# Kernel tuning notes

Hardware: AMD Instinct MI355X
Metric: run time of the kernel (lower is better)

## Reference

```python
import jax, jax.numpy as jnp
import numpy as np

NUM_HEADS = 8
EMBED_DIM = 128
HEAD_DIM = EMBED_DIM // NUM_HEADS  # 16
NB_FEATURES = EMBED_DIM            # 128
EPS = 1e-4


def _make_projection(nb_rows, nb_cols, rng):
    # gaussian_orthogonal_random_matrix with scaling=0
    blocks = []
    for _ in range(nb_rows // nb_cols):
        q, _ = np.linalg.qr(rng.standard_normal((nb_cols, nb_cols)))
        blocks.append(q.T)
    rem = nb_rows - (nb_rows // nb_cols) * nb_cols
    if rem > 0:
        q, _ = np.linalg.qr(rng.standard_normal((nb_cols, nb_cols)))
        blocks.append(q.T[:rem])
    final = np.concatenate(blocks, axis=0)
    mult = np.linalg.norm(rng.standard_normal((nb_rows, nb_cols)), axis=1)
    return (mult[:, None] * final).astype(np.float32)


def setup_inputs() -> dict:
    key = jax.random.key(0)
    ks = jax.random.split(key, 7)
    R, C, E = 8, 2048, EMBED_DIM
    s = 1.0 / np.sqrt(E)
    x = jax.random.normal(ks[0], (R, C, E), dtype=jnp.float32)
    Wq = jax.random.uniform(ks[1], (E, E), jnp.float32, -s, s)
    bq = jax.random.uniform(ks[2], (E,), jnp.float32, -s, s)
    Wk = jax.random.uniform(ks[3], (E, E), jnp.float32, -s, s)
    bk = jax.random.uniform(ks[4], (E,), jnp.float32, -s, s)
    Wv = jax.random.uniform(ks[5], (E, E), jnp.float32, -s, s)
    bv = jax.random.uniform(ks[6], (E,), jnp.float32, -s, s)
    proj = jnp.asarray(_make_projection(NB_FEATURES, HEAD_DIM, np.random.default_rng(0)))
    return {"x": x, "Wq": Wq, "bq": bq, "Wk": Wk, "bk": bk, "Wv": Wv, "bv": bv, "proj": proj}


def _softmax_kernel(data, proj, is_query):
    # data: (R, h, n, d); proj: (F, d)
    d = data.shape[-1]
    normalizer = d ** (-0.25)
    ratio = proj.shape[0] ** (-0.5)
    data_dash = jnp.einsum('rhnd,jd->rhnj', normalizer * data, proj)  # (R,h,n,F)
    diag = jnp.sum(data * data, axis=-1, keepdims=True) * 0.5 * normalizer ** 2
    if is_query:
        m = jnp.max(data_dash, axis=-1, keepdims=True)
    else:
        m = jnp.max(data_dash, axis=(-1, -2), keepdims=True)
    return ratio * (jnp.exp(data_dash - diag - m) + EPS)


def reference(x, Wq, bq, Wk, bk, Wv, bv, proj):
    R, C, E = x.shape
    h, hd = NUM_HEADS, HEAD_DIM

    def proj_heads(W, b):
        y = jnp.einsum('rce,fe->rcf', x, W) + b
        return y.reshape(R, C, h, hd).transpose(0, 2, 1, 3)  # (R,h,C,hd)

    q = _softmax_kernel(proj_heads(Wq, bq), proj, is_query=True)   # (R,h,C,F)
    k = _softmax_kernel(proj_heads(Wk, bk), proj, is_query=False)  # (R,h,C,F)
    v = proj_heads(Wv, bv)                                          # (R,h,C,hd)

    # fold batch (R) into the feature dim: (h, C, R*F) / (h, C, R*hd)
    qf = q.transpose(1, 2, 0, 3).reshape(h, C, R * NB_FEATURES)
    kf = k.transpose(1, 2, 0, 3).reshape(h, C, R * NB_FEATURES)
    vf = v.transpose(1, 2, 0, 3).reshape(h, C, R * hd)

    k_sum = kf.sum(axis=-2)                                   # (h, D)
    D_inv = 1.0 / jnp.einsum('hnd,hd->hn', qf, k_sum)         # (h, C)
    context = jnp.einsum('hnd,hne->hde', kf, vf)              # (h, D, Ev)
    out = jnp.einsum('hde,hnd,hn->hne', context, qf, D_inv)   # (h, C, R*hd)

    out = out.reshape(h, C, R, hd).transpose(2, 1, 0, 3).reshape(R, C, E)
    attn = jnp.einsum('hqf,hkf->hqk', qf, kf)                 # (h, C, C)
    return out, attn
```

## Files before the change

kernel.cpp:

```cpp
#include <hip/hip_runtime.h>
#include <hip/hip_bf16.h>
#include <stdint.h>

typedef __bf16 bf16x8 __attribute__((ext_vector_type(8)));
typedef float  f32x4  __attribute__((ext_vector_type(4)));

#define RATIO 0.08838834764831845f
#define EPSV  1e-4f

#define GLOBAL_AS __attribute__((address_space(1)))
#define LDS_AS    __attribute__((address_space(3)))

static __device__ __forceinline__ void gload16(const void* g, void* l) {
  __builtin_amdgcn_global_load_lds((GLOBAL_AS const void*)g, (LDS_AS void*)l, 16, 0, 0);
}

static constexpr size_t OFF_XB    = 0;
static constexpr size_t OFF_WCAT  = OFF_XB    + 4194304;
static constexpr size_t OFF_MQ    = OFF_WCAT  + 98304;
static constexpr size_t OFF_MK    = OFF_MQ    + 262144;
static constexpr size_t OFF_BCAT  = OFF_MK    + 262144;
static constexpr size_t OFF_BQF   = OFF_BCAT  + 2048;
static constexpr size_t OFF_BKF   = OFF_BQF   + 4096;
static constexpr size_t OFF_Y     = OFF_BKF   + 4096;
static constexpr size_t OFF_QF    = OFF_Y     + 25165824;
static constexpr size_t OFF_KF    = OFF_QF    + 33554432;
static constexpr size_t OFF_KFT   = OFF_KF    + 33554432;
static constexpr size_t OFF_VFT   = OFF_KFT   + 33554432;
static constexpr size_t OFF_KPART = OFF_VFT   + 4194304;
static constexpr size_t OFF_KMAX  = OFF_KPART + 4096;
static constexpr size_t OFF_KSPART= OFF_KMAX  + 1024;
static constexpr size_t OFF_DPART = OFF_KSPART+ 524288;
static constexpr size_t OFF_CTXP  = OFF_DPART + 524288;
static constexpr size_t OFF_CTXT  = OFF_CTXP  + 16777216;
static constexpr size_t WS_NEED   = OFF_CTXT  + 2097152;

static __device__ __forceinline__ void gemm_core(
    const __hip_bfloat16* __restrict__ A, const __hip_bfloat16* __restrict__ B,
    int lda, int ldb, int K, int tm, int tn,
    __bf16* As, __bf16* Bs, f32x4 acc[4][4]) {
  const int t    = threadIdx.x;
  const int w    = t >> 6;
  const int lane = t & 63;
  const int m_off = (w >> 1) << 6;
  const int n_off = (w & 1) << 6;
  const int r0 = t >> 2;
  const int kk = (t & 3) << 3;
  char* Asb = (char*)As + (w << 10);
  char* Bsb = (char*)Bs + (w << 10);
  const int frow = lane & 15;
  const int koff = (lane >> 4) << 3;
  for (int k0 = 0; k0 < K; k0 += 32) {
    const __hip_bfloat16* Ag = A + (size_t)(tm + r0) * lda + (k0 + kk);
    const __hip_bfloat16* Bg = B + (size_t)(tn + r0) * ldb + (k0 + kk);
    gload16(Ag, Asb);
    gload16(Ag + (size_t)64 * lda, Asb + 4096);
    gload16(Bg, Bsb);
    gload16(Bg + (size_t)64 * ldb, Bsb + 4096);
    __syncthreads();
    bf16x8 af[4], bfr[4];
#pragma unroll
    for (int mi = 0; mi < 4; ++mi)
      af[mi] = *(const bf16x8*)(As + ((m_off + mi * 16 + frow) << 5) + koff);
#pragma unroll
    for (int ni = 0; ni < 4; ++ni)
      bfr[ni] = *(const bf16x8*)(Bs + ((n_off + ni * 16 + frow) << 5) + koff);
#pragma unroll
    for (int mi = 0; mi < 4; ++mi)
#pragma unroll
      for (int ni = 0; ni < 4; ++ni)
        acc[mi][ni] = __builtin_amdgcn_mfma_f32_16x16x32_bf16(af[mi], bfr[ni], acc[mi][ni], 0, 0, 0);
    __syncthreads();
  }
}

#define ZERO_ACC(acc) do {                                   \
  _Pragma("unroll") for (int a_ = 0; a_ < 4; ++a_)           \
  _Pragma("unroll") for (int b_ = 0; b_ < 4; ++b_)           \
    acc[a_][b_] = (f32x4){0.f, 0.f, 0.f, 0.f};               \
} while (0)

__global__ void k_prep(const float* __restrict__ x,
                       const float* __restrict__ Wq, const float* __restrict__ bq,
                       const float* __restrict__ Wk, const float* __restrict__ bk,
                       const float* __restrict__ Wv, const float* __restrict__ bv,
                       const float* __restrict__ proj,
                       __hip_bfloat16* __restrict__ xb,
                       __hip_bfloat16* __restrict__ Wcat, float* __restrict__ bcat,
                       __hip_bfloat16* __restrict__ Mq, __hip_bfloat16* __restrict__ Mk,
                       float* __restrict__ bqf, float* __restrict__ bkf) {
  const int b = blockIdx.x, t = threadIdx.x;
  {
    int i = (b * 256 + t) * 4;
    f32x4 v = *(const f32x4*)(x + i);
#pragma unroll
    for (int j = 0; j < 4; ++j) xb[i + j] = __float2bfloat16(v[j]);
  }
  if (b < 1024) {
    int i = b * 256 + t;
    {
      int which = i >> 17;
      int rem = i & 131071;
      int hj = rem >> 7, e = rem & 127;
      int hh = hj >> 7, j = hj & 127;
      const float* W = which ? Wk : Wq;
      float s = 0.f;
#pragma unroll
      for (int u = 0; u < 16; ++u) s += proj[j * 16 + u] * W[(hh * 16 + u) * 128 + e];
      if (which) Mk[rem] = __float2bfloat16(0.5f * s);
      else       Mq[rem] = __float2bfloat16(0.5f * s);
    }
    if (i < 2048) {
      int which = i >> 10;
      int hj = i & 1023, hh = hj >> 7, j = hj & 127;
      const float* bb = which ? bk : bq;
      float s = 0.f;
#pragma unroll
      for (int u = 0; u < 16; ++u) s += proj[j * 16 + u] * bb[hh * 16 + u];
      if (which) bkf[hj] = 0.5f * s;
      else       bqf[hj] = 0.5f * s;
    }
  }
  if (b < 192) {
    int i = b * 256 + t;
    int mat = i >> 14, rem = i & 16383;
    const float* W = (mat == 0) ? Wq : ((mat == 1) ? Wk : Wv);
    Wcat[i] = __float2bfloat16(W[rem]);
    if (i < 384) {
      int m2 = i >> 7;
      const float* bb = (m2 == 0) ? bq : ((m2 == 1) ? bk : bv);
      bcat[i] = bb[i & 127];
    }
  }
}

__global__ __launch_bounds__(256) void k_proj(
    const __hip_bfloat16* __restrict__ xb, const __hip_bfloat16* __restrict__ Wcat,
    const float* __restrict__ bcat, float* __restrict__ Y,
    __hip_bfloat16* __restrict__ vfT) {
  __shared__ __align__(16) char pool[34816];
  __bf16* As = (__bf16*)pool;
  __bf16* Bs = (__bf16*)(pool + 8192);
  const int tm = blockIdx.x << 7, tn = blockIdx.y << 7;
  f32x4 acc[4][4];
  ZERO_ACC(acc);
  gemm_core(xb, Wcat, 128, 128, 128, tm, tn, As, Bs, acc);
  const int t = threadIdx.x, w = t >> 6, lane = t & 63;
  const int m_off = (w >> 1) << 6, n_off = (w & 1) << 6;
  const int frow = lane & 15;
  if (tn == 256) {
    __bf16* vT = (__bf16*)pool;
#pragma unroll
    for (int ni = 0; ni < 4; ++ni) {
      const int j = n_off + ni * 16 + frow;
      const float bias = bcat[256 + j];
#pragma unroll
      for (int mi = 0; mi < 4; ++mi)
#pragma unroll
        for (int i = 0; i < 4; ++i) {
          const int rl = m_off + mi * 16 + ((lane >> 4) << 2) + i;
          vT[j * 136 + rl] = (__bf16)(acc[mi][ni][i] + bias);
        }
    }
    __syncthreads();
    const int r = tm >> 11, c0 = tm & 2047;
    const int j2 = t >> 1, half = t & 1;
    const int hh = j2 >> 4, aa = j2 & 15;
    __bf16* dst = (__bf16*)vfT + (((size_t)(hh * 128 + r * 16 + aa)) << 11) + c0 + (half << 6);
    const __bf16* srcr = vT + j2 * 136 + (half << 6);
#pragma unroll
    for (int q8 = 0; q8 < 8; ++q8)
      *(bf16x8*)(dst + (q8 << 3)) = *(const bf16x8*)(srcr + (q8 << 3));
  } else {
#pragma unroll
    for (int ni = 0; ni < 4; ++ni) {
      const int col = tn + n_off + ni * 16 + frow;
      const float bias = bcat[col];
#pragma unroll
      for (int mi = 0; mi < 4; ++mi)
#pragma unroll
        for (int i = 0; i < 4; ++i) {
          const int row = tm + m_off + mi * 16 + ((lane >> 4) << 2) + i;
          Y[(size_t)row * 384 + col] = acc[mi][ni][i] + bias;
        }
    }
  }
}

__global__ __launch_bounds__(256) void k_dashk_max(
    const __hip_bfloat16* __restrict__ xb, const __hip_bfloat16* __restrict__ Mk,
    const float* __restrict__ bkf, float* __restrict__ kpart) {
  __shared__ __align__(16) __bf16 As[4096], Bs[4096];
  __shared__ float wmax[4];
  const int h = blockIdx.y;
  const int tm = blockIdx.x << 7;
  f32x4 acc[4][4];
  ZERO_ACC(acc);
  gemm_core(xb, Mk + h * 16384, 128, 128, 128, tm, 0, As, Bs, acc);
  const int t = threadIdx.x, w = t >> 6, lane = t & 63;
  const int n_off = (w & 1) << 6;
  float mx = -1e30f;
#pragma unroll
  for (int ni = 0; ni < 4; ++ni) {
    const float bia = bkf[h * 128 + n_off + ni * 16 + (lane & 15)];
#pragma unroll
    for (int mi = 0; mi < 4; ++mi)
#pragma unroll
      for (int i = 0; i < 4; ++i) mx = fmaxf(mx, acc[mi][ni][i] + bia);
  }
#pragma unroll
  for (int off = 1; off < 64; off <<= 1) mx = fmaxf(mx, __shfl_xor(mx, off));
  if (lane == 0) wmax[w] = mx;
  __syncthreads();
  if (t == 0) kpart[h * 128 + blockIdx.x] = fmaxf(fmaxf(wmax[0], wmax[1]), fmaxf(wmax[2], wmax[3]));
}

__global__ void k_kmaxred(const float* __restrict__ kpart, float* __restrict__ kmax) {
  const int t = threadIdx.x;
  const int r = t >> 3, h = t & 7;
  float m = -1e30f;
  for (int i = 0; i < 16; ++i) m = fmaxf(m, kpart[h * 128 + r * 16 + i]);
  kmax[r * 8 + h] = m;
}

__global__ __launch_bounds__(256) void k_dashk_feat(
    const __hip_bfloat16* __restrict__ xb, const __hip_bfloat16* __restrict__ Mk,
    const float* __restrict__ bkf, const float* __restrict__ Y,
    const float* __restrict__ kmax,
    __hip_bfloat16* __restrict__ kf, __hip_bfloat16* __restrict__ kfT,
    float* __restrict__ kspart) {
  __shared__ __align__(16) __bf16 As[4096], Bs[4096];
  __shared__ float diag_s[128];
  __shared__ __align__(16) __bf16 kT[128 * 136];
  __shared__ float ksp_s[2][128];
  const int h = blockIdx.y;
  const int tm = blockIdx.x << 7;
  f32x4 acc[4][4];
  ZERO_ACC(acc);
  gemm_core(xb, Mk + h * 16384, 128, 128, 128, tm, 0, As, Bs, acc);
  const int t = threadIdx.x, w = t >> 6, lane = t & 63;
  const int m_off = (w >> 1) << 6, n_off = (w & 1) << 6;
  const int frow = lane & 15;
  if (t < 128) {
    const float* yp = Y + (size_t)(tm + t) * 384 + 128 + h * 16;
    float s = 0.f;
#pragma unroll
    for (int u = 0; u < 16; ++u) s += yp[u] * yp[u];
    diag_s[t] = 0.125f * s;
  }
  const int r = tm >> 11;
  const int c0 = tm & 2047;
  const int cb = blockIdx.x & 15;
  const float m = kmax[r * 8 + h];
  float bia[4];
#pragma unroll
  for (int ni = 0; ni < 4; ++ni) bia[ni] = bkf[h * 128 + n_off + ni * 16 + frow];
  float ksp[4] = {0.f, 0.f, 0.f, 0.f};
  __syncthreads();
#pragma unroll
  for (int mi = 0; mi < 4; ++mi) {
#pragma unroll
    for (int i = 0; i < 4; ++i) {
      const int rl = m_off + mi * 16 + ((lane >> 4) << 2) + i;
      const int c = c0 + rl;
      const float dm = diag_s[rl] + m;
#pragma unroll
      for (int ni = 0; ni < 4; ++ni) {
        const int j = n_off + ni * 16 + frow;
        const float f = RATIO * (__expf(acc[mi][ni][i] + bia[ni] - dm) + EPSV);
        const __hip_bfloat16 hb = __float2bfloat16(f);
        kf[((size_t)((h << 11) + c) << 10) + (r << 7) + j] = hb;
        kT[j * 136 + rl] = (__bf16)f;
        ksp[ni] += __bfloat162float(hb);
      }
    }
  }
#pragma unroll
  for (int ni = 0; ni < 4; ++ni) {
    ksp[ni] += __shfl_xor(ksp[ni], 16);
    ksp[ni] += __shfl_xor(ksp[ni], 32);
  }
  if ((lane >> 4) == 0) {
#pragma unroll
    for (int ni = 0; ni < 4; ++ni)
      ksp_s[w >> 1][n_off + ni * 16 + frow] = ksp[ni];
  }
  __syncthreads();
  if (t < 128)
    kspart[(((cb << 3) + h) << 10) + r * 128 + t] = ksp_s[0][t] + ksp_s[1][t];
  const int j2 = t >> 1, half = t & 1;
  __bf16* dst = (__bf16*)kfT + (((size_t)(h << 10) + (r << 7) + j2) << 11) + c0 + (half << 6);
  const __bf16* srcr = kT + j2 * 136 + (half << 6);
#pragma unroll
  for (int q8 = 0; q8 < 8; ++q8)
    *(bf16x8*)(dst + (q8 << 3)) = *(const bf16x8*)(srcr + (q8 << 3));
}

__global__ __launch_bounds__(256) void k_dashq(
    const __hip_bfloat16* __restrict__ xb, const __hip_bfloat16* __restrict__ Mq,
    const float* __restrict__ bqf, const float* __restrict__ Y,
    const float* __restrict__ kspart,
    __hip_bfloat16* __restrict__ qf, float* __restrict__ dpart) {
  __shared__ __align__(16) __bf16 As[4096], Bs[4096];
  __shared__ float diag_s[128];
  __shared__ float rmax_s[2][128];
  __shared__ float ksum_s[128];
  __shared__ float dred_s[2][128];
  const int h = blockIdx.y;
  const int tm = blockIdx.x << 7;
  const int r = tm >> 11, c0 = tm & 2047;
  f32x4 acc[4][4];
  ZERO_ACC(acc);
  const int t = threadIdx.x, w = t >> 6, lane = t & 63;
  if (t < 128) {
    const float* yp = Y + (size_t)(tm + t) * 384 + h * 16;
    float s = 0.f;
#pragma unroll
    for (int u = 0; u < 16; ++u) s += yp[u] * yp[u];
    diag_s[t] = 0.125f * s;
    float ks = 0.f;
#pragma unroll
    for (int cb = 0; cb < 16; ++cb) ks += kspart[(((cb << 3) + h) << 10) + r * 128 + t];
    ksum_s[t] = ks;
  }
  gemm_core(xb, Mq + h * 16384, 128, 128, 128, tm, 0, As, Bs, acc);
  const int m_off = (w >> 1) << 6, n_off = (w & 1) << 6;
  const int frow = lane & 15;
  float bia[4];
#pragma unroll
  for (int ni = 0; ni < 4; ++ni) bia[ni] = bqf[h * 128 + n_off + ni * 16 + frow];
  float rmx[4][4];
#pragma unroll
  for (int mi = 0; mi < 4; ++mi)
#pragma unroll
    for (int i = 0; i < 4; ++i) {
      float m0 = acc[mi][0][i] + bia[0];
      m0 = fmaxf(m0, acc[mi][1][i] + bia[1]);
      m0 = fmaxf(m0, acc[mi][2][i] + bia[2]);
      m0 = fmaxf(m0, acc[mi][3][i] + bia[3]);
      rmx[mi][i] = m0;
    }
#pragma unroll
  for (int off = 1; off < 16; off <<= 1)
#pragma unroll
    for (int mi = 0; mi < 4; ++mi)
#pragma unroll
      for (int i = 0; i < 4; ++i)
        rmx[mi][i] = fmaxf(rmx[mi][i], __shfl_xor(rmx[mi][i], off));
  if (frow == 0) {
#pragma unroll
    for (int mi = 0; mi < 4; ++mi)
#pragma unroll
      for (int i = 0; i < 4; ++i)
        rmax_s[w & 1][m_off + mi * 16 + ((lane >> 4) << 2) + i] = rmx[mi][i];
  }
  __syncthreads();
  float p[4][4];
#pragma unroll
  for (int mi = 0; mi < 4; ++mi)
#pragma unroll
    for (int i = 0; i < 4; ++i) p[mi][i] = 0.f;
#pragma unroll
  for (int mi = 0; mi < 4; ++mi) {
#pragma unroll
    for (int i = 0; i < 4; ++i) {
      const int rl = m_off + mi * 16 + ((lane >> 4) << 2) + i;
      const float md = diag_s[rl] + fmaxf(rmax_s[0][rl], rmax_s[1][rl]);
#pragma unroll
      for (int ni = 0; ni < 4; ++ni) {
        const int j = n_off + ni * 16 + frow;
        const float f = RATIO * (__expf(acc[mi][ni][i] + bia[ni] - md) + EPSV);
        const __hip_bfloat16 hb = __float2bfloat16(f);
        qf[((size_t)((h << 11) + c0 + rl) << 10) + (r << 7) + j] = hb;
        p[mi][i] += __bfloat162float(hb) * ksum_s[j];
      }
    }
  }
#pragma unroll
  for (int off = 1; off < 16; off <<= 1)
#pragma unroll
    for (int mi = 0; mi < 4; ++mi)
#pragma unroll
      for (int i = 0; i < 4; ++i)
        p[mi][i] += __shfl_xor(p[mi][i], off);
  if (frow == 0) {
#pragma unroll
    for (int mi = 0; mi < 4; ++mi)
#pragma unroll
      for (int i = 0; i < 4; ++i)
        dred_s[w & 1][m_off + mi * 16 + ((lane >> 4) << 2) + i] = p[mi][i];
  }
  __syncthreads();
  if (t < 128)
    dpart[(((r << 3) + h) << 11) + c0 + t] = dred_s[0][t] + dred_s[1][t];
}

#define SBAR() __builtin_amdgcn_s_barrier()
#define FEN()  do { asm volatile("" ::: "memory"); __builtin_amdgcn_sched_barrier(0); } while (0)
#define PRIO1() __builtin_amdgcn_s_setprio(1)
#define PRIO0() __builtin_amdgcn_s_setprio(0)
#define VMW4() do { asm volatile("s_waitcnt vmcnt(4)" ::: "memory"); } while (0)
#define VMW0() do { asm volatile("s_waitcnt vmcnt(0)" ::: "memory"); } while (0)

#define MFMA16(nlo) do {                                                      \
  _Pragma("unroll") for (int mi_ = 0; mi_ < 8; ++mi_)                         \
  _Pragma("unroll") for (int nj_ = 0; nj_ < 2; ++nj_)                         \
    acc[mi_][(nlo) + nj_] = __builtin_amdgcn_mfma_f32_16x16x32_bf16(          \
        aR[mi_], bR[nj_], acc[mi_][(nlo) + nj_], 0, 0, 0);                    \
} while (0)

__global__ __launch_bounds__(512, 2) void k_attn8(
    const __hip_bfloat16* __restrict__ qf, const __hip_bfloat16* __restrict__ kf,
    float* __restrict__ attn) {
  extern __shared__ __align__(128) char lds[];
  const int lid = blockIdx.x;
  const int swz = ((lid & 7) << 6) + (lid >> 3);
  const int h  = swz >> 6;
  const int tm = ((swz >> 3) & 7) << 8;
  const int tn = (swz & 7) << 8;
  const __hip_bfloat16* Ag = qf + ((size_t)h << 21);
  const __hip_bfloat16* Bg = kf + ((size_t)h << 21);

  const int t = threadIdx.x, wid = t >> 6, lane = t & 63;
  const int f = lane & 15;
  const int wr = wid >> 2, wc = wid & 3;
  const int swzg = (((lane >> 4) ^ ((f >> 1) & 3)) << 4);
  const int aoff = ((wr << 7) + f) * 64 + swzg;
  const int boff = 65536 + ((wc << 6) + f) * 64 + swzg;
  const int srow = t >> 2;
  const int scol = (((t & 3) ^ ((t >> 3) & 3)) << 3);
  const int sdst = wid << 10;

  f32x4 acc[8][4] = {};
  bf16x8 aR[8], bR[2];

  auto stageA = [&](int buf, int kh, int k0) {
    char* d = lds + buf * 32768 + kh * 16384 + sdst;
    const __hip_bfloat16* g = Ag + (size_t)(tm + srow) * 1024 + k0 + (kh << 5) + scol;
    gload16(g, d);
    gload16(g + 128 * 1024, d + 8192);
  };
  auto stageB = [&](int buf, int kh, int k0) {
    char* d = lds + 65536 + buf * 32768 + kh * 16384 + sdst;
    const __hip_bfloat16* g = Bg + (size_t)(tn + srow) * 1024 + k0 + (kh << 5) + scol;
    gload16(g, d);
    gload16(g + 128 * 1024, d + 8192);
  };

  stageA(0, 0, 0); stageB(0, 0, 0); stageA(0, 1, 0); stageB(0, 1, 0);
  VMW4();
  SBAR(); FEN();

  for (int kt = 0; kt < 15; ++kt) {
    const int buf = kt & 1, nbuf = buf ^ 1;
    const int bo = buf * 32768;
    const int nk0 = (kt + 1) << 6;
#pragma unroll
    for (int mi = 0; mi < 8; ++mi) aR[mi] = *(const bf16x8*)(lds + bo + aoff + mi * 1024);
    bR[0] = *(const bf16x8*)(lds + bo + boff);
    bR[1] = *(const bf16x8*)(lds + bo + boff + 1024);
    stageA(nbuf, 0, nk0);
    PRIO1(); MFMA16(0); PRIO0();
    SBAR(); FEN();
    bR[0] = *(const bf16x8*)(lds + bo + boff + 2048);
    bR[1] = *(const bf16x8*)(lds + bo + boff + 3072);
    stageB(nbuf, 0, nk0);
    PRIO1(); MFMA16(2); PRIO0();
    VMW4();
    SBAR(); FEN();
#pragma unroll
    for (int mi = 0; mi < 8; ++mi) aR[mi] = *(const bf16x8*)(lds + bo + 16384 + aoff + mi * 1024);
    bR[0] = *(const bf16x8*)(lds + bo + 16384 + boff);
    bR[1] = *(const bf16x8*)(lds + bo + 16384 + boff + 1024);
    stageA(nbuf, 1, nk0);
    PRIO1(); MFMA16(0); PRIO0();
    SBAR(); FEN();
    bR[0] = *(const bf16x8*)(lds + bo + 16384 + boff + 2048);
    bR[1] = *(const bf16x8*)(lds + bo + 16384 + boff + 3072);
    stageB(nbuf, 1, nk0);
    PRIO1(); MFMA16(2); PRIO0();
    VMW4();
    SBAR(); FEN();
  }
  {
    const int bo = 32768;
#pragma unroll
    for (int mi = 0; mi < 8; ++mi) aR[mi] = *(const bf16x8*)(lds + bo + aoff + mi * 1024);
    bR[0] = *(const bf16x8*)(lds + bo + boff);
    bR[1] = *(const bf16x8*)(lds + bo + boff + 1024);
    PRIO1(); MFMA16(0); PRIO0();
    bR[0] = *(const bf16x8*)(lds + bo + boff + 2048);
    bR[1] = *(const bf16x8*)(lds + bo + boff + 3072);
    PRIO1(); MFMA16(2); PRIO0();
    VMW0();
    SBAR(); FEN();
#pragma unroll
    for (int mi = 0; mi < 8; ++mi) aR[mi] = *(const bf16x8*)(lds + bo + 16384 + aoff + mi * 1024);
    bR[0] = *(const bf16x8*)(lds + bo + 16384 + boff);
    bR[1] = *(const bf16x8*)(lds + bo + 16384 + boff + 1024);
    PRIO1(); MFMA16(0); PRIO0();
    bR[0] = *(const bf16x8*)(lds + bo + 16384 + boff + 2048);
    bR[1] = *(const bf16x8*)(lds + bo + 16384 + boff + 3072);
    PRIO1(); MFMA16(2); PRIO0();
  }

  float* Cc = attn + ((size_t)h << 22);
  const int rbase = tm + (wr << 7) + ((lane >> 4) << 2);
  const int cbase = tn + (wc << 6) + f;
#pragma unroll
  for (int mi = 0; mi < 8; ++mi)
#pragma unroll
    for (int i = 0; i < 4; ++i) {
      float* rp = Cc + ((size_t)(rbase + mi * 16 + i) << 11) + cbase;
#pragma unroll
      for (int ni = 0; ni < 4; ++ni) rp[ni * 16] = acc[mi][ni][i];
    }
}

__global__ __launch_bounds__(256) void k_ctx(
    const __hip_bfloat16* __restrict__ vfT, const __hip_bfloat16* __restrict__ kfT,
    float* __restrict__ ctxp) {
  __shared__ __align__(16) __bf16 As[4096], Bs[4096];
  const int z = blockIdx.z, h = z >> 2, kc = z & 3;
  const int tn = blockIdx.y << 7;
  f32x4 acc[4][4];
  ZERO_ACC(acc);
  gemm_core(vfT + ((size_t)h << 18) + (kc << 9), kfT + ((size_t)h << 21) + (kc << 9),
            2048, 2048, 512, 0, tn, As, Bs, acc);
  float* Cp = ctxp + ((size_t)(kc * 8 + h) << 17);
  const int t = threadIdx.x, w = t >> 6, lane = t & 63;
  const int m_off = (w >> 1) << 6, n_off = (w & 1) << 6;
#pragma unroll
  for (int mi = 0; mi < 4; ++mi)
#pragma unroll
    for (int i = 0; i < 4; ++i) {
      const int row = m_off + mi * 16 + ((lane >> 4) << 2) + i;
#pragma unroll
      for (int ni = 0; ni < 4; ++ni) {
        const int col = tn + n_off + ni * 16 + (lane & 15);
        Cp[((size_t)row << 10) + col] = acc[mi][ni][i];
      }
    }
}

__global__ void k_ctxred(const float* __restrict__ ctxp, __hip_bfloat16* __restrict__ ctxT) {
  const int i = blockIdx.x * 256 + threadIdx.x;
  const float s = ctxp[i] + ctxp[i + 1048576] + ctxp[i + 2097152] + ctxp[i + 3145728];
  ctxT[i] = __float2bfloat16(s);
}

__global__ __launch_bounds__(256) void k_out(
    const __hip_bfloat16* __restrict__ qf, const __hip_bfloat16* __restrict__ ctxT,
    const float* __restrict__ dpart, float* __restrict__ outp) {
  __shared__ __align__(16) __bf16 As[4096], Bs[4096];
  __shared__ float dinv_s[128];
  const int h = blockIdx.z;
  const int tm = blockIdx.x << 7;
  const int t = threadIdx.x, w = t >> 6, lane = t & 63;
  if (t < 128) {
    float s = 0.f;
#pragma unroll
    for (int r = 0; r < 8; ++r) s += dpart[(((r << 3) + h) << 11) + tm + t];
    dinv_s[t] = 1.0f / s;
  }
  f32x4 acc[4][4];
  ZERO_ACC(acc);
  gemm_core(qf + ((size_t)h << 21), ctxT + ((size_t)h << 17), 1024, 1024, 1024, tm, 0, As, Bs, acc);
  const int m_off = (w >> 1) << 6, n_off = (w & 1) << 6;
#pragma unroll
  for (int mi = 0; mi < 4; ++mi)
#pragma unroll
    for (int i = 0; i < 4; ++i) {
      const int rl = m_off + mi * 16 + ((lane >> 4) << 2) + i;
      const int row = tm + rl;
      const float dv = dinv_s[rl];
#pragma unroll
      for (int ni = 0; ni < 4; ++ni) {
        const int col = n_off + ni * 16 + (lane & 15);
        const int rb = col >> 4, tt = col & 15;
        outp[(((size_t)(rb << 11) + row) << 7) + (h << 4) + tt] = acc[mi][ni][i] * dv;
      }
    }
}

extern "C" void kernel_launch(void* const* d_in, const int* in_sizes, int n_in,
                              void* d_out, int out_size, void* d_ws, size_t ws_size,
                              hipStream_t stream) {
  const float* x    = (const float*)d_in[0];
  const float* Wq   = (const float*)d_in[1];
  const float* bq   = (const float*)d_in[2];
  const float* Wk   = (const float*)d_in[3];
  const float* bk   = (const float*)d_in[4];
  const float* Wv   = (const float*)d_in[5];
  const float* bv   = (const float*)d_in[6];
  const float* proj = (const float*)d_in[7];
  if (ws_size < WS_NEED) return;

  char* ws = (char*)d_ws;
  __hip_bfloat16* xb   = (__hip_bfloat16*)(ws + OFF_XB);
  __hip_bfloat16* Wcat = (__hip_bfloat16*)(ws + OFF_WCAT);
  __hip_bfloat16* Mq   = (__hip_bfloat16*)(ws + OFF_MQ);
  __hip_bfloat16* Mk   = (__hip_bfloat16*)(ws + OFF_MK);
  float* bcat = (float*)(ws + OFF_BCAT);
  float* bqf  = (float*)(ws + OFF_BQF);
  float* bkf  = (float*)(ws + OFF_BKF);
  float* Y    = (float*)(ws + OFF_Y);
  __hip_bfloat16* qf  = (__hip_bfloat16*)(ws + OFF_QF);
  __hip_bfloat16* kf  = (__hip_bfloat16*)(ws + OFF_KF);
  __hip_bfloat16* kfT = (__hip_bfloat16*)(ws + OFF_KFT);
  __hip_bfloat16* vfT = (__hip_bfloat16*)(ws + OFF_VFT);
  float* kpart  = (float*)(ws + OFF_KPART);
  float* kmax   = (float*)(ws + OFF_KMAX);
  float* kspart = (float*)(ws + OFF_KSPART);
  float* dpart  = (float*)(ws + OFF_DPART);
  float* ctxp   = (float*)(ws + OFF_CTXP);
  __hip_bfloat16* ctxT = (__hip_bfloat16*)(ws + OFF_CTXT);

  float* outp = (float*)d_out;
  float* attn = (float*)d_out + 2097152;

  static int attr_done = 0;
  if (!attr_done) {
    (void)hipFuncSetAttribute((const void*)k_attn8,
                              hipFuncAttributeMaxDynamicSharedMemorySize, 131072);
    attr_done = 1;
  }

  k_prep<<<dim3(2048), dim3(256), 0, stream>>>(x, Wq, bq, Wk, bk, Wv, bv, proj,
                                               xb, Wcat, bcat, Mq, Mk, bqf, bkf);
  k_proj<<<dim3(128, 3), dim3(256), 0, stream>>>(xb, Wcat, bcat, Y, vfT);
  k_dashk_max<<<dim3(128, 8), dim3(256), 0, stream>>>(xb, Mk, bkf, kpart);
  k_kmaxred<<<dim3(1), dim3(64), 0, stream>>>(kpart, kmax);
  k_dashk_feat<<<dim3(128, 8), dim3(256), 0, stream>>>(xb, Mk, bkf, Y, kmax, kf, kfT, kspart);
  k_dashq<<<dim3(128, 8), dim3(256), 0, stream>>>(xb, Mq, bqf, Y, kspart, qf, dpart);
  k_attn8<<<dim3(512), dim3(512), 131072, stream>>>(qf, kf, attn);
  k_ctx<<<dim3(1, 8, 32), dim3(256), 0, stream>>>(vfT, kfT, ctxp);
  k_ctxred<<<dim3(4096), dim3(256), 0, stream>>>(ctxp, ctxT);
  k_out<<<dim3(16, 1, 8), dim3(256), 0, stream>>>(qf, ctxT, dpart, outp);
}
```

Baseline: 191.1 us.

## Fuse kmax reduction, drop attn barriers, vectorize ctxred, retile out GEMM

Result: faster. 183.6 us (-3.9%).

```diff
diff --git a/kernel.cpp b/kernel.cpp
--- a/kernel.cpp
+++ b/kernel.cpp
@@ -3,6 +3,7 @@
 #include <stdint.h>
 
 typedef __bf16 bf16x8 __attribute__((ext_vector_type(8)));
+typedef __bf16 bf16x4 __attribute__((ext_vector_type(4)));
 typedef float  f32x4  __attribute__((ext_vector_type(4)));
 
 #define RATIO 0.08838834764831845f
@@ -215,18 +216,10 @@
   if (t == 0) kpart[h * 128 + blockIdx.x] = fmaxf(fmaxf(wmax[0], wmax[1]), fmaxf(wmax[2], wmax[3]));
 }
 
-__global__ void k_kmaxred(const float* __restrict__ kpart, float* __restrict__ kmax) {
-  const int t = threadIdx.x;
-  const int r = t >> 3, h = t & 7;
-  float m = -1e30f;
-  for (int i = 0; i < 16; ++i) m = fmaxf(m, kpart[h * 128 + r * 16 + i]);
-  kmax[r * 8 + h] = m;
-}
-
 __global__ __launch_bounds__(256) void k_dashk_feat(
     const __hip_bfloat16* __restrict__ xb, const __hip_bfloat16* __restrict__ Mk,
     const float* __restrict__ bkf, const float* __restrict__ Y,
-    const float* __restrict__ kmax,
+    const float* __restrict__ kpart,
     __hip_bfloat16* __restrict__ kf, __hip_bfloat16* __restrict__ kfT,
     float* __restrict__ kspart) {
   __shared__ __align__(16) __bf16 As[4096], Bs[4096];
@@ -251,7 +244,12 @@
   const int r = tm >> 11;
   const int c0 = tm & 2047;
   const int cb = blockIdx.x & 15;
-  const float m = kmax[r * 8 + h];
+  float m = -1e30f;
+  {
+    const float* kp = kpart + h * 128 + r * 16;
+#pragma unroll
+    for (int i = 0; i < 16; ++i) m = fmaxf(m, kp[i]);
+  }
   float bia[4];
 #pragma unroll
   for (int ni = 0; ni < 4; ++ni) bia[ni] = bkf[h * 128 + n_off + ni * 16 + frow];
@@ -461,7 +459,6 @@
     bR[1] = *(const bf16x8*)(lds + bo + boff + 1024);
     stageA(nbuf, 0, nk0);
     PRIO1(); MFMA16(0); PRIO0();
-    SBAR(); FEN();
     bR[0] = *(const bf16x8*)(lds + bo + boff + 2048);
     bR[1] = *(const bf16x8*)(lds + bo + boff + 3072);
     stageB(nbuf, 0, nk0);
@@ -474,7 +471,6 @@
     bR[1] = *(const bf16x8*)(lds + bo + 16384 + boff + 1024);
     stageA(nbuf, 1, nk0);
     PRIO1(); MFMA16(0); PRIO0();
-    SBAR(); FEN();
     bR[0] = *(const bf16x8*)(lds + bo + 16384 + boff + 2048);
     bR[1] = *(const bf16x8*)(lds + bo + 16384 + boff + 3072);
     stageB(nbuf, 1, nk0);
@@ -544,31 +540,66 @@
 }
 
 __global__ void k_ctxred(const float* __restrict__ ctxp, __hip_bfloat16* __restrict__ ctxT) {
-  const int i = blockIdx.x * 256 + threadIdx.x;
-  const float s = ctxp[i] + ctxp[i + 1048576] + ctxp[i + 2097152] + ctxp[i + 3145728];
-  ctxT[i] = __float2bfloat16(s);
-}
-
-__global__ __launch_bounds__(256) void k_out(
+  const int i = (blockIdx.x * 256 + threadIdx.x) * 4;
+  f32x4 a = *(const f32x4*)(ctxp + i);
+  f32x4 b = *(const f32x4*)(ctxp + i + 1048576);
+  f32x4 c = *(const f32x4*)(ctxp + i + 2097152);
+  f32x4 d = *(const f32x4*)(ctxp + i + 3145728);
+  bf16x4 o;
+#pragma unroll
+  for (int j = 0; j < 4; ++j) o[j] = (__bf16)(a[j] + b[j] + c[j] + d[j]);
+  *(bf16x4*)((__bf16*)ctxT + i) = o;
+}
+
+__global__ __launch_bounds__(256) void k_out64(
     const __hip_bfloat16* __restrict__ qf, const __hip_bfloat16* __restrict__ ctxT,
     const float* __restrict__ dpart, float* __restrict__ outp) {
-  __shared__ __align__(16) __bf16 As[4096], Bs[4096];
-  __shared__ float dinv_s[128];
+  __shared__ __align__(16) __bf16 As[2048], Bs[4096];
+  __shared__ float dinv_s[64];
   const int h = blockIdx.z;
-  const int tm = blockIdx.x << 7;
+  const int tm = blockIdx.x << 6;
   const int t = threadIdx.x, w = t >> 6, lane = t & 63;
-  if (t < 128) {
+  if (t < 64) {
     float s = 0.f;
 #pragma unroll
     for (int r = 0; r < 8; ++r) s += dpart[(((r << 3) + h) << 11) + tm + t];
     dinv_s[t] = 1.0f / s;
   }
-  f32x4 acc[4][4];
-  ZERO_ACC(acc);
-  gemm_core(qf + ((size_t)h << 21), ctxT + ((size_t)h << 17), 1024, 1024, 1024, tm, 0, As, Bs, acc);
-  const int m_off = (w >> 1) << 6, n_off = (w & 1) << 6;
-#pragma unroll
-  for (int mi = 0; mi < 4; ++mi)
+  const int m_off = (w >> 1) << 5, n_off = (w & 1) << 6;
+  const int r0 = t >> 2, kk = (t & 3) << 3;
+  char* Asb = (char*)As + ((t >> 6) << 10);
+  char* Bsb = (char*)Bs + ((t >> 6) << 10);
+  const int frow = lane & 15, koff = (lane >> 4) << 3;
+  const __hip_bfloat16* A = qf + ((size_t)h << 21);
+  const __hip_bfloat16* B = ctxT + ((size_t)h << 17);
+  f32x4 acc[2][4];
+#pragma unroll
+  for (int a_ = 0; a_ < 2; ++a_)
+#pragma unroll
+    for (int b_ = 0; b_ < 4; ++b_) acc[a_][b_] = (f32x4){0.f, 0.f, 0.f, 0.f};
+  for (int k0 = 0; k0 < 1024; k0 += 32) {
+    const __hip_bfloat16* Agp = A + (size_t)(tm + r0) * 1024 + (k0 + kk);
+    const __hip_bfloat16* Bgp = B + (size_t)r0 * 1024 + (k0 + kk);
+    gload16(Agp, Asb);
+    gload16(Bgp, Bsb);
+    gload16(Bgp + (size_t)64 * 1024, Bsb + 4096);
+    __syncthreads();
+    bf16x8 af[2], bfr[4];
+#pragma unroll
+    for (int mi = 0; mi < 2; ++mi)
+      af[mi] = *(const bf16x8*)(As + ((m_off + mi * 16 + frow) << 5) + koff);
+#pragma unroll
+    for (int ni = 0; ni < 4; ++ni)
+      bfr[ni] = *(const bf16x8*)(Bs + ((n_off + ni * 16 + frow) << 5) + koff);
+#pragma unroll
+    for (int mi = 0; mi < 2; ++mi)
+#pragma unroll
+      for (int ni = 0; ni < 4; ++ni)
+        acc[mi][ni] = __builtin_amdgcn_mfma_f32_16x16x32_bf16(af[mi], bfr[ni], acc[mi][ni], 0, 0, 0);
+    __syncthreads();
+  }
+#pragma unroll
+  for (int mi = 0; mi < 2; ++mi)
 #pragma unroll
     for (int i = 0; i < 4; ++i) {
       const int rl = m_off + mi * 16 + ((lane >> 4) << 2) + i;
@@ -576,7 +607,7 @@
       const float dv = dinv_s[rl];
 #pragma unroll
       for (int ni = 0; ni < 4; ++ni) {
-        const int col = n_off + ni * 16 + (lane & 15);
+        const int col = n_off + ni * 16 + frow;
         const int rb = col >> 4, tt = col & 15;
         outp[(((size_t)(rb << 11) + row) << 7) + (h << 4) + tt] = acc[mi][ni][i] * dv;
       }
@@ -610,7 +641,6 @@
   __hip_bfloat16* kfT = (__hip_bfloat16*)(ws + OFF_KFT);
   __hip_bfloat16* vfT = (__hip_bfloat16*)(ws + OFF_VFT);
   float* kpart  = (float*)(ws + OFF_KPART);
-  float* kmax   = (float*)(ws + OFF_KMAX);
   float* kspart = (float*)(ws + OFF_KSPART);
   float* dpart  = (float*)(ws + OFF_DPART);
   float* ctxp   = (float*)(ws + OFF_CTXP);
@@ -630,11 +660,10 @@
                                                xb, Wcat, bcat, Mq, Mk, bqf, bkf);
   k_proj<<<dim3(128, 3), dim3(256), 0, stream>>>(xb, Wcat, bcat, Y, vfT);
   k_dashk_max<<<dim3(128, 8), dim3(256), 0, stream>>>(xb, Mk, bkf, kpart);
-  k_kmaxred<<<dim3(1), dim3(64), 0, stream>>>(kpart, kmax);
-  k_dashk_feat<<<dim3(128, 8), dim3(256), 0, stream>>>(xb, Mk, bkf, Y, kmax, kf, kfT, kspart);
+  k_dashk_feat<<<dim3(128, 8), dim3(256), 0, stream>>>(xb, Mk, bkf, Y, kpart, kf, kfT, kspart);
   k_dashq<<<dim3(128, 8), dim3(256), 0, stream>>>(xb, Mq, bqf, Y, kspart, qf, dpart);
   k_attn8<<<dim3(512), dim3(512), 131072, stream>>>(qf, kf, attn);
   k_ctx<<<dim3(1, 8, 32), dim3(256), 0, stream>>>(vfT, kfT, ctxp);
-  k_ctxred<<<dim3(4096), dim3(256), 0, stream>>>(ctxp, ctxT);
-  k_out<<<dim3(16, 1, 8), dim3(256), 0, stream>>>(qf, ctxT, dpart, outp);
-}
+  k_ctxred<<<dim3(1024), dim3(256), 0, stream>>>(ctxp, ctxT);
+  k_out64<<<dim3(32, 1, 8), dim3(256), 0, stream>>>(qf, ctxT, dpart, outp);
+}
```
